# Optimization experiments

Measured on AMD Instinct MI355X. Metric: run time of the kernel, lower is better.

## Reference

```python
import jax, jax.numpy as jnp
import numpy as np


def setup_inputs() -> dict:
    key = jax.random.key(0)
    k1, k2 = jax.random.split(key)
    z = jax.random.normal(k1, (16, 128, 32, 32), dtype=jnp.float32)
    codes = jax.random.normal(k2, (8, 512, 16), dtype=jnp.float32)  # [latent_dim, num_codes, channel_dim]
    return {"z": z, "codes": codes}


def reference(z, codes):
    L, K, D = codes.shape          # latent_dim, num_codes, channel_dim
    B, C, H, W = z.shape           # C == L * D
    # permute to channels-last and split channels into (L, D)
    h = jnp.transpose(z, (0, 2, 3, 1)).reshape(B, H, W, L, D)
    # pairwise L2 distances via ||h||^2 - 2 h.W + ||W||^2 (avoids materializing [B,H,W,L,K,D])
    h2 = jnp.sum(h * h, axis=-1)                      # [B,H,W,L]
    w2 = jnp.sum(codes * codes, axis=-1)              # [L,K]
    cross = jnp.einsum('bhwld,lkd->bhwlk', h, codes)  # [B,H,W,L,K]
    d2 = h2[..., None] - 2.0 * cross + w2[None, None, None]
    distances = jnp.sqrt(jnp.maximum(d2, 1e-12))      # [B,H,W,L,K]
    # softmin over codes == softmax of negated distances
    probs = jax.nn.softmax(-distances, axis=4)
    soft_symbols = jnp.einsum('bhwlk,lkd->bhwld', probs, codes).reshape(B, H, W, C)
    # hard assignment: nearest code per latent dim
    idxes = jnp.argmin(distances, axis=4)             # [B,H,W,L]
    hard_symbols = codes[jnp.arange(L), idxes]        # [B,H,W,L,D]
    hard_symbols = hard_symbols.reshape(B, H, W, C)
    return (soft_symbols, hard_symbols, idxes)
```

## Files before the change

### kernel.cpp

```cpp
#include <hip/hip_runtime.h>
#include <hip/hip_bf16.h>

typedef float  f32x4  __attribute__((ext_vector_type(4)));
typedef short  s16x8  __attribute__((ext_vector_type(8)));
typedef __bf16 bf16x8 __attribute__((ext_vector_type(8)));

namespace {
constexpr int BHW = 16384, L = 8, K = 512, D = 16, HW = 1024, CH = 128;
constexpr int TPB = 512;
constexpr int PPB = 256;
constexpr float KAPPA = 2.0813689810056077f;
constexpr size_t WS_CA_BYTES = (size_t)L * K * 32 * 2;
constexpr size_t WS_W2_BYTES = (size_t)L * K * 4;
constexpr size_t WS_W2K_OFF  = WS_CA_BYTES + WS_W2_BYTES;

__device__ __forceinline__ f32x4 mfma16(s16x8 a, s16x8 b, f32x4 c) {
  return __builtin_amdgcn_mfma_f32_16x16x32_bf16(
      __builtin_bit_cast(bf16x8, a), __builtin_bit_cast(bf16x8, b), c, 0, 0, 0);
}
__device__ __forceinline__ unsigned short bfh(float x) {
  return __builtin_bit_cast(unsigned short, __float2bfloat16(x));
}
__device__ __forceinline__ float bf2f(unsigned short u) {
  return __bfloat162float(__builtin_bit_cast(__hip_bfloat16, u));
}

__global__ void repack(const float* __restrict__ codes,
                       unsigned short* __restrict__ cA,
                       float* __restrict__ w2g, float* __restrict__ w2k) {
  int i = blockIdx.x * 256 + threadIdx.x;
  const float* c = codes + (size_t)i * D;
  float s = 0.f;
  #pragma unroll
  for (int d = 0; d < D; ++d) s = fmaf(c[d], c[d], s);
  w2g[i] = s;
  w2k[i] = KAPPA * s;
  int l = i >> 9, k = i & (K - 1);
  int ck = k >> 5, kloc = k & 31, g = kloc >> 3, w = kloc & 7, t = w >> 2, r = w & 3;
  int prow = ck * 32 + t * 16 + g * 4 + r;
  unsigned short* dst = cA + ((size_t)l * K + prow) * 32;
  #pragma unroll
  for (int d = 0; d < D; ++d) {
    unsigned short hi = bfh(c[d]);
    dst[d] = hi; dst[16 + d] = bfh(c[d] - bf2f(hi));
  }
}

__global__ __launch_bounds__(TPB, 4) void enc_mfma(
    const float* __restrict__ z,
    const float* __restrict__ codes,
    const unsigned short* __restrict__ cA,
    const float* __restrict__ w2g,
    const float* __restrict__ w2k,
    float* __restrict__ out)
{
  __shared__ short cB[2][8192];
  __shared__ float w2s[K];
  __shared__ float h2s[PPB];
  __shared__ float ssum[8][32];
  __shared__ int   bks[8][32];

  const int tid  = threadIdx.x;
  const int l    = blockIdx.y;
  const int bx   = blockIdx.x;
  const int bimg = bx >> 2;
  const int yx0  = (bx & 3) * PPB;

  float* hstg = (float*)&cB[0][0];
  {
    const int i = tid & 255, dc = tid >> 8;
    #pragma unroll
    for (int it = 0; it < 8; ++it) {
      int d = dc * 8 + it;
      hstg[i * 17 + d] = z[((size_t)(bimg * CH + l * D + d)) * HW + yx0 + i];
    }
  }
  __syncthreads();

  const int wv   = __builtin_amdgcn_readfirstlane(tid >> 6);
  const int lane = tid & 63;
  const int cl   = lane & 15;
  const int g    = lane >> 4;
  const int pw   = wv * 32;

  if (tid < PPB) {
    float h2 = 0.f;
    #pragma unroll
    for (int d = 0; d < 16; ++d) { float v = hstg[tid * 17 + d]; h2 = fmaf(v, v, h2); }
    h2s[tid] = h2;
  }
  s16x8 B1a, B2a, B1b, B2b;
  {
    const int off = (g & 1) * 8;
    #pragma unroll
    for (int j = 0; j < 8; ++j) {
      float va = hstg[(pw + cl) * 17 + off + j];
      unsigned short ha = bfh(va);
      B1a[j] = (short)ha; B2a[j] = (short)bfh(va - bf2f(ha));
      float vb = hstg[(pw + 16 + cl) * 17 + off + j];
      unsigned short hb = bfh(vb);
      B1b[j] = (short)hb; B2b[j] = (short)bfh(vb - bf2f(hb));
    }
  }
  __syncthreads();
  const float h2ka = KAPPA * h2s[pw + cl];
  const float h2kb = KAPPA * h2s[pw + 16 + cl];

  {
    int k = tid, ck = k >> 5, kloc = k & 31, gg = kloc >> 3, w = kloc & 7, t = w >> 2, r = w & 3;
    int prow = ck * 32 + t * 16 + gg * 4 + r;
    const s16x8* src = (const s16x8*)(cA + ((size_t)l * K + prow) * 32);
    s16x8 h0 = src[0], h1 = src[1], l0 = src[2], l1 = src[3];
    int base = (ck * 4 + gg) * 128 + w;
    #pragma unroll
    for (int d = 0; d < 8; ++d) {
      cB[0][base + d * 8]       = h0[d];
      cB[1][base + d * 8]       = l0[d];
      cB[0][base + (d + 8) * 8] = h1[d];
      cB[1][base + (d + 8) * 8] = l1[d];
    }
    w2s[k] = w2k[l * K + k];
  }
  __syncthreads();

  const s16x8* Ab = (const s16x8*)(cA + (size_t)l * K * 32) + (cl * 4 + g);
  const s16x8 ONES = {(short)0x3F80, (short)0x3F80, (short)0x3F80, (short)0x3F80,
                      (short)0x3F80, (short)0x3F80, (short)0x3F80, (short)0x3F80};

  float m2A = 1e30f, mbA = 1e30f;
  float m2B = 1e30f, mbB = 1e30f;
  f32x4 pva0 = {0,0,0,0}, pva1 = {0,0,0,0}, pvsA = {0,0,0,0};
  f32x4 pvb0 = {0,0,0,0}, pvb1 = {0,0,0,0}, pvsB = {0,0,0,0};

  auto soft8 = [&](const f32x4& T0, const f32x4& T1, const f32x4& W0, const f32x4& W1,
                   float h2k, int ct, float& m2, float& m2b) -> s16x8 {
    s16x8 PA;
    #pragma unroll
    for (int t = 0; t < 2; ++t) {
      #pragma unroll
      for (int r = 0; r < 4; ++r) {
        float T  = t ? T1[r] : T0[r];
        float Wk = t ? W1[r] : W0[r];
        float d2 = fmaf(-2.f * KAPPA, T, h2k) + Wk;
        d2 = fmaxf(d2, 1e-12f);
        int kloc = ct * 32 + 8 * g + t * 4 + r;
        float key = __int_as_float((__float_as_int(d2) & 0xFFFFFE00) | kloc);
        m2b = __builtin_amdgcn_fmed3f(key, m2, m2b);
        m2  = fminf(m2, key);
        float dist = __builtin_amdgcn_sqrtf(d2);
        float w = __builtin_amdgcn_exp2f(-dist);
        PA[t * 4 + r] = (short)bfh(w);
      }
    }
    return PA;
  };

  f32x4 T0a_p = {0,0,0,0}, T1a_p = {0,0,0,0}, T0b_p = {0,0,0,0}, T1b_p = {0,0,0,0};
  {
    s16x8 A0 = Ab[0], A1 = Ab[64];
    __builtin_amdgcn_s_setprio(1);
    T0a_p = mfma16(A0, B1a, T0a_p); T0a_p = mfma16(A0, B2a, T0a_p);
    T1a_p = mfma16(A1, B1a, T1a_p); T1a_p = mfma16(A1, B2a, T1a_p);
    T0b_p = mfma16(A0, B1b, T0b_p); T0b_p = mfma16(A0, B2b, T0b_p);
    T1b_p = mfma16(A1, B1b, T1b_p); T1b_p = mfma16(A1, B2b, T1b_p);
    __builtin_amdgcn_s_setprio(0);
  }

  #pragma unroll 2
  for (int ct = 0; ct < 16; ++ct) {
    f32x4 T0a_c = {0,0,0,0}, T1a_c = {0,0,0,0}, T0b_c = {0,0,0,0}, T1b_c = {0,0,0,0};
    if (ct < 15) {
      s16x8 A0 = Ab[(ct + 1) * 128], A1 = Ab[(ct + 1) * 128 + 64];
      __builtin_amdgcn_s_setprio(1);
      T0a_c = mfma16(A0, B1a, T0a_c); T0a_c = mfma16(A0, B2a, T0a_c);
      T1a_c = mfma16(A1, B1a, T1a_c); T1a_c = mfma16(A1, B2a, T1a_c);
      T0b_c = mfma16(A0, B1b, T0b_c); T0b_c = mfma16(A0, B2b, T0b_c);
      T1b_c = mfma16(A1, B1b, T1b_c); T1b_c = mfma16(A1, B2b, T1b_c);
      __builtin_amdgcn_s_setprio(0);
    }
    s16x8 Bh = *(const s16x8*)&cB[0][(ct * 4 + g) * 128 + cl * 8];
    s16x8 Bl = *(const s16x8*)&cB[1][(ct * 4 + g) * 128 + cl * 8];
    f32x4 W0 = *(const f32x4*)&w2s[ct * 32 + 8 * g];
    f32x4 W1 = *(const f32x4*)&w2s[ct * 32 + 8 * g + 4];

    s16x8 PAa = soft8(T0a_p, T1a_p, W0, W1, h2ka, ct, m2A, mbA);
    s16x8 PAb = soft8(T0b_p, T1b_p, W0, W1, h2kb, ct, m2B, mbB);
    __builtin_amdgcn_s_setprio(1);
    pva0 = mfma16(PAa, Bh, pva0); pva1 = mfma16(PAa, Bl, pva1); pvsA = mfma16(PAa, ONES, pvsA);
    pvb0 = mfma16(PAb, Bh, pvb0); pvb1 = mfma16(PAb, Bl, pvb1); pvsB = mfma16(PAb, ONES, pvsB);
    __builtin_amdgcn_s_setprio(0);
    T0a_p = T0a_c; T1a_p = T1a_c; T0b_p = T0b_c; T1b_p = T1b_c;
  }
  f32x4 pva = pva0 + pva1;
  f32x4 pvb = pvb0 + pvb1;

  #pragma unroll
  for (int off = 16; off < 64; off <<= 1) {
    float mo = __shfl_xor(m2A, off), mbo = __shfl_xor(mbA, off);
    mbA = fminf(fminf(mbA, mbo), fmaxf(m2A, mo));
    m2A = fminf(m2A, mo);
    float mo2 = __shfl_xor(m2B, off), mbo2 = __shfl_xor(mbB, off);
    mbB = fminf(fminf(mbB, mbo2), fmaxf(m2B, mo2));
    m2B = fminf(m2B, mo2);
  }
  int kaA = __float_as_int(m2A) & 511;
  int kaB = __float_as_int(m2B) & 511;
  bool trigA = (__int_as_float(__float_as_int(mbA) & 0xFFFFFE00) -
                __int_as_float(__float_as_int(m2A) & 0xFFFFFE00)) < 0.045f;
  bool trigB = (__int_as_float(__float_as_int(mbB) & 0xFFFFFE00) -
                __int_as_float(__float_as_int(m2B) & 0xFFFFFE00)) < 0.045f;

  if (cl == 0) {
    #pragma unroll
    for (int r = 0; r < 4; ++r) {
      ssum[wv][g * 4 + r]      = pvsA[r];
      ssum[wv][16 + g * 4 + r] = pvsB[r];
    }
  }
  if (lane < 16) { bks[wv][lane] = kaA; bks[wv][16 + lane] = kaB; }

  unsigned long long mask = __ballot(lane < 16 && trigA) |
                            (__ballot(lane < 16 && trigB) << 16);
  while (mask) {
    int pl = __ffsll((long long)mask) - 1; mask &= mask - 1;
    float hh[16];
    #pragma unroll
    for (int d = 0; d < 16; ++d)
      hh[d] = z[((size_t)(bimg * CH + l * D + d)) * HW + yx0 + pw + pl];
    float h2x = h2s[pw + pl];
    float bm = 1e30f; int bkk = 0;
    for (int rnd = 0; rnd < 8; ++rnd) {
      int k = rnd * 64 + lane;
      const float* cr = codes + ((size_t)l * K + k) * D;
      float cross = 0.f;
      #pragma unroll
      for (int d = 0; d < 16; ++d) cross = fmaf(hh[d], cr[d], cross);
      float d2 = (h2x - 2.f * cross) + w2g[l * K + k];
      d2 = fmaxf(d2, 1e-12f);
      float dist = sqrtf(d2);
      if (dist < bm) { bm = dist; bkk = k; }
    }
    #pragma unroll
    for (int off = 1; off < 64; off <<= 1) {
      float bo = __shfl_xor(bm, off); int ko = __shfl_xor(bkk, off);
      if (bo < bm || (bo == bm && ko < bkk)) { bm = bo; bkk = ko; }
    }
    if (lane == 0) bks[wv][pl] = bkk;
  }

  __syncthreads();
  const int pg0 = bimg * HW + yx0;
  f32x4 svA = *(const f32x4*)&ssum[wv][g * 4];
  f32x4 svB = *(const f32x4*)&ssum[wv][16 + g * 4];
  #pragma unroll
  for (int r = 0; r < 4; ++r) {
    out[(size_t)(pg0 + pw + g * 4 + r) * CH + l * D + cl]      = pva[r] * __builtin_amdgcn_rcpf(svA[r]);
    out[(size_t)(pg0 + pw + 16 + g * 4 + r) * CH + l * D + cl] = pvb[r] * __builtin_amdgcn_rcpf(svB[r]);
  }
  int kkA = bks[wv][cl];
  int kkB = bks[wv][16 + cl];
  float4 cvA = *(const float4*)&codes[((size_t)l * K + kkA) * D + g * 4];
  float4 cvB = *(const float4*)&codes[((size_t)l * K + kkB) * D + g * 4];
  *(float4*)&out[(size_t)BHW * CH + (size_t)(pg0 + pw + cl) * CH + l * D + g * 4]      = cvA;
  *(float4*)&out[(size_t)BHW * CH + (size_t)(pg0 + pw + 16 + cl) * CH + l * D + g * 4] = cvB;
  if (lane < 16) {
    out[(size_t)2 * BHW * CH + (size_t)(pg0 + pw + cl) * L + l]      = (float)kkA;
    out[(size_t)2 * BHW * CH + (size_t)(pg0 + pw + 16 + cl) * L + l] = (float)kkB;
  }
}
}

extern "C" void kernel_launch(void* const* d_in, const int* in_sizes, int n_in,
                              void* d_out, int out_size, void* d_ws, size_t ws_size,
                              hipStream_t stream) {
  const float* z     = (const float*)d_in[0];
  const float* codes = (const float*)d_in[1];
  float* out         = (float*)d_out;
  unsigned short* cA = (unsigned short*)d_ws;
  float* w2g         = (float*)((char*)d_ws + WS_CA_BYTES);
  float* w2k         = (float*)((char*)d_ws + WS_W2K_OFF);

  repack<<<dim3(L * K / 256), 256, 0, stream>>>(codes, cA, w2g, w2k);
  dim3 grid(BHW / PPB, L);
  enc_mfma<<<grid, TPB, 0, stream>>>(z, codes, cA, w2g, w2k, out);
}
```

Measured before the change: 63.75 us.

## Stage per-latent code matrix in LDS and drop software-pipelined MFMA prefetch

Each block now copies the 32 KB split-bf16 code matrix for its latent dim into a new shared-memory array up front, and the main loop reads the MFMA A operands from LDS instead of global memory. The one-tile-ahead software pipeline of the distance MFMAs is removed; the distance MFMAs are now issued in the same iteration as the softmax and PV MFMAs. This removes global-load latency from the inner loop and cuts register pressure from the carried accumulators, but raises LDS use per block by 32 KB, which may lower occupancy below the launch-bounds target, and it loses the overlap between MFMA and the VALU softmax work.

```diff
diff --git a/kernel.cpp b/kernel.cpp
--- a/kernel.cpp
+++ b/kernel.cpp
@@ -55,6 +55,7 @@
     float* __restrict__ out)
 {
   __shared__ short cB[2][8192];
+  __shared__ short cAl[16384];
   __shared__ float w2s[K];
   __shared__ float h2s[PPB];
   __shared__ float ssum[8][32];
@@ -74,6 +75,11 @@
       int d = dc * 8 + it;
       hstg[i * 17 + d] = z[((size_t)(bimg * CH + l * D + d)) * HW + yx0 + i];
     }
+  }
+  {
+    const s16x8* src = (const s16x8*)(cA + ((size_t)l * K + tid) * 32);
+    s16x8* dst = (s16x8*)cAl + tid * 4;
+    dst[0] = src[0]; dst[1] = src[1]; dst[2] = src[2]; dst[3] = src[3];
   }
   __syncthreads();
 
@@ -123,7 +129,7 @@
   }
   __syncthreads();
 
-  const s16x8* Ab = (const s16x8*)(cA + (size_t)l * K * 32) + (cl * 4 + g);
+  const s16x8* Abl = (const s16x8*)cAl + (cl * 4 + g);
   const s16x8 ONES = {(short)0x3F80, (short)0x3F80, (short)0x3F80, (short)0x3F80,
                       (short)0x3F80, (short)0x3F80, (short)0x3F80, (short)0x3F80};
 
@@ -155,41 +161,29 @@
     return PA;
   };
 
-  f32x4 T0a_p = {0,0,0,0}, T1a_p = {0,0,0,0}, T0b_p = {0,0,0,0}, T1b_p = {0,0,0,0};
-  {
-    s16x8 A0 = Ab[0], A1 = Ab[64];
-    __builtin_amdgcn_s_setprio(1);
-    T0a_p = mfma16(A0, B1a, T0a_p); T0a_p = mfma16(A0, B2a, T0a_p);
-    T1a_p = mfma16(A1, B1a, T1a_p); T1a_p = mfma16(A1, B2a, T1a_p);
-    T0b_p = mfma16(A0, B1b, T0b_p); T0b_p = mfma16(A0, B2b, T0b_p);
-    T1b_p = mfma16(A1, B1b, T1b_p); T1b_p = mfma16(A1, B2b, T1b_p);
-    __builtin_amdgcn_s_setprio(0);
-  }
-
   #pragma unroll 2
   for (int ct = 0; ct < 16; ++ct) {
-    f32x4 T0a_c = {0,0,0,0}, T1a_c = {0,0,0,0}, T0b_c = {0,0,0,0}, T1b_c = {0,0,0,0};
-    if (ct < 15) {
-      s16x8 A0 = Ab[(ct + 1) * 128], A1 = Ab[(ct + 1) * 128 + 64];
-      __builtin_amdgcn_s_setprio(1);
-      T0a_c = mfma16(A0, B1a, T0a_c); T0a_c = mfma16(A0, B2a, T0a_c);
-      T1a_c = mfma16(A1, B1a, T1a_c); T1a_c = mfma16(A1, B2a, T1a_c);
-      T0b_c = mfma16(A0, B1b, T0b_c); T0b_c = mfma16(A0, B2b, T0b_c);
-      T1b_c = mfma16(A1, B1b, T1b_c); T1b_c = mfma16(A1, B2b, T1b_c);
-      __builtin_amdgcn_s_setprio(0);
-    }
+    s16x8 A0 = Abl[ct * 128];
+    s16x8 A1 = Abl[ct * 128 + 64];
     s16x8 Bh = *(const s16x8*)&cB[0][(ct * 4 + g) * 128 + cl * 8];
     s16x8 Bl = *(const s16x8*)&cB[1][(ct * 4 + g) * 128 + cl * 8];
     f32x4 W0 = *(const f32x4*)&w2s[ct * 32 + 8 * g];
     f32x4 W1 = *(const f32x4*)&w2s[ct * 32 + 8 * g + 4];
 
-    s16x8 PAa = soft8(T0a_p, T1a_p, W0, W1, h2ka, ct, m2A, mbA);
-    s16x8 PAb = soft8(T0b_p, T1b_p, W0, W1, h2kb, ct, m2B, mbB);
+    f32x4 T0a = {0,0,0,0}, T1a = {0,0,0,0}, T0b = {0,0,0,0}, T1b = {0,0,0,0};
+    __builtin_amdgcn_s_setprio(1);
+    T0a = mfma16(A0, B1a, T0a); T0a = mfma16(A0, B2a, T0a);
+    T1a = mfma16(A1, B1a, T1a); T1a = mfma16(A1, B2a, T1a);
+    T0b = mfma16(A0, B1b, T0b); T0b = mfma16(A0, B2b, T0b);
+    T1b = mfma16(A1, B1b, T1b); T1b = mfma16(A1, B2b, T1b);
+    __builtin_amdgcn_s_setprio(0);
+
+    s16x8 PAa = soft8(T0a, T1a, W0, W1, h2ka, ct, m2A, mbA);
+    s16x8 PAb = soft8(T0b, T1b, W0, W1, h2kb, ct, m2B, mbB);
     __builtin_amdgcn_s_setprio(1);
     pva0 = mfma16(PAa, Bh, pva0); pva1 = mfma16(PAa, Bl, pva1); pvsA = mfma16(PAa, ONES, pvsA);
     pvb0 = mfma16(PAb, Bh, pvb0); pvb1 = mfma16(PAb, Bl, pvb1); pvsB = mfma16(PAb, ONES, pvsB);
     __builtin_amdgcn_s_setprio(0);
-    T0a_p = T0a_c; T1a_p = T1a_c; T0b_p = T0b_c; T1b_p = T1b_c;
   }
   f32x4 pva = pva0 + pva1;
   f32x4 pvb = pvb0 + pvb1;
```

New measurement: 61.24 us. -3.9%, faster.
